# Kernel optimization log

Measured on AMD Instinct MI355X. Metric: run time of the kernel, lower is better.

Reference implementation:

```python
import jax, jax.numpy as jnp
import numpy as np

N_QUBITS = 6
N_LAYERS = 3
DIM = 2 ** N_QUBITS  # 64
BATCH = 262144
FEATURE_DIM = 4
HIDDEN_DIM = 16
N_CLASSES = 4
N_QW = N_LAYERS * N_QUBITS * 3  # 54


def _apply_1q(state, gate, q):
    """Apply a single-qubit gate to qubit q (little-endian: qubit 0 = LSB).
    state: [B, DIM] complex64. gate: [2,2] (shared) or [B,2,2] (per-sample)."""
    B = state.shape[0]
    st = state.reshape(B, 2 ** (N_QUBITS - 1 - q), 2, 2 ** q)
    if gate.ndim == 2:
        out = jnp.einsum('ij,bkjl->bkil', gate, st)
    else:
        out = jnp.einsum('bij,bkjl->bkil', gate, st)
    return out.reshape(B, DIM)


def _cx_perm(c, t):
    # CX(control=c, target=t) is a permutation of basis states: flip bit t where bit c is 1.
    idx = np.arange(DIM)
    return jnp.asarray(idx ^ (((idx >> c) & 1) << t))


def _ry_batched(theta):  # theta: [B] -> [B,2,2]
    c = jnp.cos(theta / 2).astype(jnp.complex64)
    s = jnp.sin(theta / 2).astype(jnp.complex64)
    return jnp.stack([jnp.stack([c, -s], -1), jnp.stack([s, c], -1)], -2)


def _rx(t):  # scalar angle -> [2,2]
    c = jnp.cos(t / 2).astype(jnp.complex64)
    s = jnp.sin(t / 2).astype(jnp.complex64)
    return jnp.stack([jnp.stack([c, -1j * s]), jnp.stack([-1j * s, c])]).astype(jnp.complex64)


def _ry(t):
    c = jnp.cos(t / 2).astype(jnp.complex64)
    s = jnp.sin(t / 2).astype(jnp.complex64)
    return jnp.stack([jnp.stack([c, -s]), jnp.stack([s, c])]).astype(jnp.complex64)


def _rz(t):
    e_m = jnp.exp(-0.5j * t).astype(jnp.complex64)
    e_p = jnp.exp(0.5j * t).astype(jnp.complex64)
    z = jnp.zeros((), jnp.complex64)
    return jnp.stack([jnp.stack([e_m, z]), jnp.stack([z, e_p])])


_H = (jnp.array([[1, 1], [1, -1]], jnp.float32) / np.float32(np.sqrt(2.0))).astype(jnp.complex64)
# signs[s, q] = +1 if bit q of basis state s is 0, else -1  -> Z expectation via probs @ signs
_SIGNS = jnp.asarray(
    1.0 - 2.0 * ((np.arange(DIM)[:, None] >> np.arange(N_QUBITS)[None, :]) & 1),
    dtype=jnp.float32)


def quantum_expectations(angles, qw):
    """Exact batched statevector simulation of the parameterized circuit.
    angles: [B, N_QUBITS] input-encoding RY angles; qw: [N_QW] variational params.
    Returns per-qubit Z expectations [B, N_QUBITS] (exact, i.e. infinite-shot limit)."""
    B = angles.shape[0]
    state = jnp.zeros((B, DIM), jnp.complex64).at[:, 0].set(1.0)
    # Encoding: H then RY(x_q) on each qubit
    for q in range(N_QUBITS):
        state = _apply_1q(state, _H, q)
        state = _apply_1q(state, _ry_batched(angles[:, q]), q)
    # Variational layers
    p = 0
    for _layer in range(N_LAYERS):
        for q in range(N_QUBITS - 1):
            state = state[:, _cx_perm(q, q + 1)]
        for q in range(N_QUBITS):
            state = _apply_1q(state, _rx(qw[p]), q); p += 1
            state = _apply_1q(state, _ry(qw[p]), q); p += 1
            state = _apply_1q(state, _rz(qw[p]), q); p += 1
    probs = state.real ** 2 + state.imag ** 2  # [B, DIM]
    return probs @ _SIGNS  # [B, N_QUBITS]


def setup_inputs() -> dict:
    key = jax.random.key(0)
    ks = jax.random.split(key, 10)
    d = {
        'x': jax.random.normal(ks[0], (BATCH, FEATURE_DIM), jnp.float32),
        'pre_w1': jax.random.normal(ks[1], (FEATURE_DIM, HIDDEN_DIM), jnp.float32) * 0.3,
        'pre_b1': jnp.zeros((HIDDEN_DIM,), jnp.float32),
        'pre_w2': jax.random.normal(ks[2], (HIDDEN_DIM, N_QUBITS), jnp.float32) * 0.2,
        'pre_b2': jnp.zeros((N_QUBITS,), jnp.float32),
        'qw': jax.random.normal(ks[3], (N_QW,), jnp.float32) * 0.1,
        'post_w1': jax.random.normal(ks[4], (N_QUBITS, HIDDEN_DIM), jnp.float32) * 0.3,
        'post_b1': jnp.zeros((HIDDEN_DIM,), jnp.float32),
        'post_w2': jax.random.normal(ks[5], (HIDDEN_DIM, N_CLASSES), jnp.float32) * 0.2,
        'post_b2': jnp.zeros((N_CLASSES,), jnp.float32),
    }
    return d


def reference(x, pre_w1, pre_b1, pre_w2, pre_b2, qw, post_w1, post_b1, post_w2, post_b2):
    # classical_preprocess (dropout is identity in eval): Linear -> ReLU -> Linear -> Tanh
    h = jax.nn.relu(x @ pre_w1 + pre_b1)
    angles = jnp.tanh(h @ pre_w2 + pre_b2)  # [B, N_QUBITS]
    # quantum circuit (original detaches inputs before the circuit -> no grad through it)
    exp = jax.lax.stop_gradient(quantum_expectations(angles, qw))
    # classical_postprocess: Linear -> ReLU -> Linear
    h2 = jax.nn.relu(exp @ post_w1 + post_b1)
    return h2 @ post_w2 + post_b2
```

## Files before the change

### kernel.cpp

```cpp
#include <hip/hip_runtime.h>
#include <math.h>

#define NQ 6
#define NLAYERS 3
#define QBATCH 262144
#define NGATES 18
#define GSTRIDE 40

typedef float  f2   __attribute__((ext_vector_type(2)));
typedef float  f4v  __attribute__((ext_vector_type(4)));
typedef float  f16f __attribute__((ext_vector_type(16)));
typedef __fp16 h2v  __attribute__((ext_vector_type(2)));
typedef __fp16 h8v  __attribute__((ext_vector_type(8)));

__device__ __forceinline__ float lane_swap(float v) {
    return __int_as_float(__builtin_amdgcn_update_dpp(
        0, __float_as_int(v), 0xB1, 0xF, 0xF, true));
}
__device__ __forceinline__ f2 lane_swap2(f2 v) {
    f2 r; r.x = lane_swap(v.x); r.y = lane_swap(v.y); return r;
}
__device__ __forceinline__ float tanh_fast(float a) {
    const float e = __expf(2.f * a);
    return 1.f - 2.f * __builtin_amdgcn_rcpf(e + 1.f);
}

__global__ __launch_bounds__(128) void prep_kernel(
    const float* __restrict__ qw,
    const float* __restrict__ post_w1,
    __fp16* __restrict__ wfrag)
{
    __shared__ f2    gs2[NGATES * GSTRIDE / 2];
    __shared__ float Ure[64][65];
    __shared__ float Uim[64][65];
    const int tid = threadIdx.x;

    if (tid < NGATES) {
        const int pp = tid * 3;
        float s0 = sinf(qw[pp+0]*0.5f), c0 = cosf(qw[pp+0]*0.5f);
        float s1 = sinf(qw[pp+1]*0.5f), c1 = cosf(qw[pp+1]*0.5f);
        float s2 = sinf(qw[pp+2]*0.5f), c2 = cosf(qw[pp+2]*0.5f);
        const float m00r =  c1*c0, m00i =  s1*s0;
        const float m01r = -s1*c0, m01i = -c1*s0;
        const float m10r =  s1*c0, m10i = -c1*s0;
        const float m11r =  c1*c0, m11i = -s1*s0;
        const float g00r = c2*m00r + s2*m00i, g00i = c2*m00i - s2*m00r;
        const float g01r = c2*m01r + s2*m01i, g01i = c2*m01i - s2*m01r;
        const float g10r = c2*m10r - s2*m10i, g10i = c2*m10i + s2*m10r;
        const float g11r = c2*m11r - s2*m11i, g11i = c2*m11i + s2*m11r;
        float* o = (float*)gs2 + tid * GSTRIDE;
        o[0]=o[1]=g00r;  o[2]=o[3]=g00i;  o[4]=o[5]=-g00i;
        o[6]=o[7]=g01r;  o[8]=o[9]=g01i;  o[10]=o[11]=-g01i;
        o[12]=o[13]=g10r; o[14]=o[15]=g10i; o[16]=o[17]=-g10i;
        o[18]=o[19]=g11r; o[20]=o[21]=g11i; o[22]=o[23]=-g11i;
        o[24]=g00r; o[25]=g10r;  o[26]=g00i; o[27]=g10i;
        o[28]=-g00i; o[29]=-g10i; o[30]=g01r; o[31]=g11r;
        o[32]=g01i; o[33]=g11i;  o[34]=-g01i; o[35]=-g11i;
        o[36]=o[37]=o[38]=o[39]=0.f;
    }
    __syncthreads();

    {
        const int bt = tid >> 1, p = tid & 1;
        f2 R[16], U[16];
        #pragma unroll
        for (int j = 0; j < 16; ++j) {
            R[j].x = ((bt >> 5) == p && (bt & 31) == 2*j    ) ? 1.f : 0.f;
            R[j].y = ((bt >> 5) == p && (bt & 31) == 2*j + 1) ? 1.f : 0.f;
            U[j].x = 0.f; U[j].y = 0.f;
        }
        const f2* gpack = gs2;
        #pragma unroll 1
        for (int l = 0; l < NLAYERS; ++l) {
            #pragma unroll
            for (int j = 0; j < 16; j += 2) {
                float t;
                t = R[j].y; R[j].y = R[j+1].y; R[j+1].y = t;
                t = U[j].y; U[j].y = U[j+1].y; U[j+1].y = t;
            }
            #pragma unroll
            for (int c = 1; c < 4; ++c) {
                #pragma unroll
                for (int j = 0; j < 16; ++j) {
                    if (((j >> (c-1)) & 1) && !((j >> c) & 1)) {
                        const int t = j | (1 << c);
                        f2 tmp;
                        tmp = R[j]; R[j] = R[t]; R[t] = tmp;
                        tmp = U[j]; U[j] = U[t]; U[t] = tmp;
                    }
                }
            }
            #pragma unroll
            for (int j = 8; j < 16; ++j) {
                R[j] = lane_swap2(R[j]);
                U[j] = lane_swap2(U[j]);
            }
            const f2* lg = gpack + l * (NQ * (GSTRIDE / 2));
            {
                const f2* gb = lg;
                const f2 A = gb[12], Ai = gb[13], nAi = gb[14];
                const f2 C = gb[15], Ci = gb[16], nCi = gb[17];
                #pragma unroll
                for (int j = 0; j < 16; ++j) {
                    const f2 z = R[j], u = U[j];
                    const f2 br0 = __builtin_shufflevector(z, z, 0, 0);
                    const f2 br1 = __builtin_shufflevector(z, z, 1, 1);
                    const f2 bu0 = __builtin_shufflevector(u, u, 0, 0);
                    const f2 bu1 = __builtin_shufflevector(u, u, 1, 1);
                    R[j] = __builtin_elementwise_fma(nCi, bu1, __builtin_elementwise_fma(C,  br1, __builtin_elementwise_fma(nAi, bu0, A  * br0)));
                    U[j] = __builtin_elementwise_fma(C,   bu1, __builtin_elementwise_fma(Ci, br1, __builtin_elementwise_fma(A,   bu0, Ai * br0)));
                }
            }
            #pragma unroll
            for (int q = 1; q < 5; ++q) {
                const f2* gb = lg + q * (GSTRIDE / 2);
                const f2 a00r = gb[0], a00i = gb[1],  n00i = gb[2];
                const f2 a01r = gb[3], a01i = gb[4],  n01i = gb[5];
                const f2 a10r = gb[6], a10i = gb[7],  n10i = gb[8];
                const f2 a11r = gb[9], a11i = gb[10], n11i = gb[11];
                const int bit = 1 << (q - 1);
                #pragma unroll
                for (int m = 0; m < 8; ++m) {
                    const int ja = ((m >> (q-1)) << q) | (m & (bit - 1));
                    const int jb = ja | bit;
                    const f2 zr0 = R[ja], zu0 = U[ja];
                    const f2 zr1 = R[jb], zu1 = U[jb];
                    R[ja] = __builtin_elementwise_fma(n01i, zu1, __builtin_elementwise_fma(a01r, zr1, __builtin_elementwise_fma(n00i, zu0, a00r * zr0)));
                    U[ja] = __builtin_elementwise_fma(a01r, zu1, __builtin_elementwise_fma(a01i, zr1, __builtin_elementwise_fma(a00r, zu0, a00i * zr0)));
                    R[jb] = __builtin_elementwise_fma(n11i, zu1, __builtin_elementwise_fma(a11r, zr1, __builtin_elementwise_fma(n10i, zu0, a10r * zr0)));
                    U[jb] = __builtin_elementwise_fma(a11r, zu1, __builtin_elementwise_fma(a11i, zr1, __builtin_elementwise_fma(a10r, zu0, a10i * zr0)));
                }
            }
            {
                const f2* gb = lg + 5 * (GSTRIDE / 2);
                const bool sw = (p != 0);
                const f2 rrr  = sw ? gb[9]  : gb[0];
                const f2 rri  = sw ? gb[10] : gb[1];
                const f2 nrri = sw ? gb[11] : gb[2];
                const f2 rpr  = sw ? gb[6]  : gb[3];
                const f2 rpi  = sw ? gb[7]  : gb[4];
                const f2 nrpi = sw ? gb[8]  : gb[5];
                #pragma unroll
                for (int j = 0; j < 16; ++j) {
                    const f2 z = R[j], u = U[j];
                    const f2 pr = lane_swap2(z), pu = lane_swap2(u);
                    R[j] = __builtin_elementwise_fma(nrpi, pu, __builtin_elementwise_fma(rpr, pr, __builtin_elementwise_fma(nrri, u, rrr * z)));
                    U[j] = __builtin_elementwise_fma(rpr,  pu, __builtin_elementwise_fma(rpi, pr, __builtin_elementwise_fma(rrr,  u, rri * z)));
                }
            }
        }
        #pragma unroll
        for (int j = 0; j < 16; ++j) {
            Ure[32*p + 2*j    ][bt] = R[j].x;
            Ure[32*p + 2*j + 1][bt] = R[j].y;
            Uim[32*p + 2*j    ][bt] = U[j].x;
            Uim[32*p + 2*j + 1][bt] = U[j].y;
        }
    }
    __syncthreads();

    {
        const int lane = tid & 63, w = tid >> 6;
        const int r32 = lane & 31, kh = lane >> 5;
        for (int i = w; i < 16; i += 2) {
            const int T = i >> 2, s = i & 3;
            const int row = 32*T + r32, n = row >> 1, cmp = row & 1;
            const float* src = cmp ? &Uim[n][0] : &Ure[n][0];
            h8v v;
            #pragma unroll
            for (int e = 0; e < 8; ++e) v[e] = (__fp16)src[kh*8 + 16*s + e];
            *(h8v*)(wfrag + i*512 + lane*8) = v;
        }
        if (w == 0) {
            const int rlow = lane & 15, kg = lane >> 4;
            float cw[6];
            #pragma unroll
            for (int q = 0; q < 6; ++q) cw[q] = post_w1[q*16 + rlow];
            for (int f = 0; f < 2; ++f) {
                h8v v;
                #pragma unroll
                for (int e = 0; e < 8; ++e) {
                    const int k2 = kg*8 + e + 32*f;
                    float sacc = 0.f;
                    #pragma unroll
                    for (int q = 0; q < 6; ++q)
                        sacc += ((k2 >> q) & 1) ? -cw[q] : cw[q];
                    v[e] = (__fp16)sacc;
                }
                *(h8v*)(wfrag + 8192 + f*512 + lane*8) = v;
            }
        }
    }
}

__global__ __launch_bounds__(256) void qnn_mfma_kernel(
    const float* __restrict__ x,
    const float* __restrict__ pre_w1, const float* __restrict__ pre_b1,
    const float* __restrict__ pre_w2, const float* __restrict__ pre_b2,
    const __fp16* __restrict__ wfrag,
    const float* __restrict__ post_b1, const float* __restrict__ post_w2,
    const float* __restrict__ post_b2,
    float* __restrict__ out)
{
    __shared__ __align__(16) __fp16 ps[4][2048];
    const int tid  = threadIdx.x;
    const int lane = tid & 63, wid = tid >> 6;
    const int sbase = (blockIdx.x * 4 + wid) * 64;

    h8v a1f[16];
    #pragma unroll
    for (int i = 0; i < 16; ++i)
        a1f[i] = *(const h8v*)(wfrag + i*512 + lane*8);
    const h8v a2f0 = *(const h8v*)(wfrag + 8192 + lane*8);
    const h8v a2f1 = *(const h8v*)(wfrag + 8192 + 512 + lane*8);

    const float4 xv = ((const float4*)x)[sbase + lane];
    float h[16];
    #pragma unroll
    for (int j = 0; j < 16; ++j) {
        float a = pre_b1[j];
        a = fmaf(xv.x, pre_w1[0*16+j], a);
        a = fmaf(xv.y, pre_w1[1*16+j], a);
        a = fmaf(xv.z, pre_w1[2*16+j], a);
        a = fmaf(xv.w, pre_w1[3*16+j], a);
        h[j] = fmaxf(a, 0.f);
    }
    float fc[NQ], fs[NQ];
    #pragma unroll
    for (int q = 0; q < NQ; ++q) {
        float a = pre_b2[q];
        #pragma unroll
        for (int j = 0; j < 16; ++j) a = fmaf(h[j], pre_w2[j*NQ+q], a);
        const float y = 0.5f * tanh_fast(a) + 0.78539816339744831f;
        fc[q] = __cosf(y); fs[q] = __sinf(y);
    }
    const float b2x = post_b2[0], b2y = post_b2[1];
    const float b2z = post_b2[2], b2w = post_b2[3];

    const int sl32 = lane & 31, kh = lane >> 5;
    const int sl16 = lane & 15, g2 = lane >> 4;
    __fp16* myp = ps[wid];
    const int wswz = (sl32 & 7) << 4;

    #pragma unroll
    for (int G2 = 0; G2 < 2; ++G2) {
        const int srcb = (G2 * 32 + sl32) << 2;
        #define BP(v) __int_as_float(__builtin_amdgcn_ds_bpermute(srcb, __float_as_int(v)))
        const float q0c=BP(fc[0]), q0s=BP(fs[0]);
        const float q1c=BP(fc[1]), q1s=BP(fs[1]);
        const float q2c=BP(fc[2]), q2s=BP(fs[2]);
        const float q3c=BP(fc[3]), q3s=BP(fs[3]);
        const float q4c=BP(fc[4]), q4s=BP(fs[4]);
        const float q5c=BP(fc[5]), q5s=BP(fs[5]);
        #undef BP
        const float f3v = kh ? q3s : q3c;
        float t01[4], b8[8];
        t01[0] = q0c*q1c; t01[1] = q0s*q1c; t01[2] = q0c*q1s; t01[3] = q0s*q1s;
        #pragma unroll
        for (int e = 0; e < 8; ++e) b8[e] = t01[e & 3] * ((e & 4) ? q2s : q2c);
        h8v bs[4];
        #pragma unroll
        for (int s = 0; s < 4; ++s) {
            const float pre = f3v * ((s & 1) ? q4s : q4c) * ((s & 2) ? q5s : q5c);
            #pragma unroll
            for (int e2 = 0; e2 < 4; ++e2) {
                const h2v t = __builtin_amdgcn_cvt_pkrtz(b8[2*e2]*pre, b8[2*e2+1]*pre);
                bs[s][2*e2] = t[0]; bs[s][2*e2+1] = t[1];
            }
        }

        f16f acc[4];
        #pragma unroll
        for (int T = 0; T < 4; ++T) acc[T] = (f16f)(0.f);
        #pragma unroll
        for (int s = 0; s < 4; ++s) {
            #pragma unroll
            for (int T = 0; T < 4; ++T)
                acc[T] = __builtin_amdgcn_mfma_f32_32x32x16_f16(
                    a1f[T*4 + s], bs[s], acc[T], 0, 0, 0);
        }

        #pragma unroll
        for (int T = 0; T < 4; ++T) {
            #pragma unroll
            for (int a = 0; a < 4; ++a) {
                const float p0 = fmaf(acc[T][4*a+0], acc[T][4*a+0],
                                      acc[T][4*a+1] * acc[T][4*a+1]);
                const float p1 = fmaf(acc[T][4*a+2], acc[T][4*a+2],
                                      acc[T][4*a+3] * acc[T][4*a+3]);
                const h2v ph = __builtin_amdgcn_cvt_pkrtz(p0, p1);
                const int boff = (32*T + 8*a + 4*kh) ^ wswz;
                *(h2v*)((char*)myp + sl32*128 + boff) = ph;
            }
        }

        #pragma unroll
        for (int H = 0; H < 2; ++H) {
            const int smp  = H*16 + sl16;
            const int rswz = (smp & 7) << 4;
            const h8v pb0 = *(const h8v*)((const char*)myp + smp*128 + ((16*g2     ) ^ rswz));
            const h8v pb1 = *(const h8v*)((const char*)myp + smp*128 + ((16*g2 + 64) ^ rswz));
            f4v c2 = {0.f, 0.f, 0.f, 0.f};
            c2 = __builtin_amdgcn_mfma_f32_16x16x32_f16(a2f0, pb0, c2, 0, 0, 0);
            c2 = __builtin_amdgcn_mfma_f32_16x16x32_f16(a2f1, pb1, c2, 0, 0, 0);

            const float4 b1v = ((const float4*)post_b1)[g2];
            const float e0  = fmaxf(c2.x + b1v.x, 0.f);
            const float e1  = fmaxf(c2.y + b1v.y, 0.f);
            const float e2_ = fmaxf(c2.z + b1v.z, 0.f);
            const float e3  = fmaxf(c2.w + b1v.w, 0.f);
            const float4 w0 = ((const float4*)post_w2)[4*g2 + 0];
            const float4 w1 = ((const float4*)post_w2)[4*g2 + 1];
            const float4 w2 = ((const float4*)post_w2)[4*g2 + 2];
            const float4 w3 = ((const float4*)post_w2)[4*g2 + 3];
            float ox = fmaf(e0, w0.x, fmaf(e1, w1.x, fmaf(e2_, w2.x, e3 * w3.x)));
            float oy = fmaf(e0, w0.y, fmaf(e1, w1.y, fmaf(e2_, w2.y, e3 * w3.y)));
            float oz = fmaf(e0, w0.z, fmaf(e1, w1.z, fmaf(e2_, w2.z, e3 * w3.z)));
            float ow = fmaf(e0, w0.w, fmaf(e1, w1.w, fmaf(e2_, w2.w, e3 * w3.w)));
            ox += __shfl_xor(ox, 16, 64); ox += __shfl_xor(ox, 32, 64);
            oy += __shfl_xor(oy, 16, 64); oy += __shfl_xor(oy, 32, 64);
            oz += __shfl_xor(oz, 16, 64); oz += __shfl_xor(oz, 32, 64);
            ow += __shfl_xor(ow, 16, 64); ow += __shfl_xor(ow, 32, 64);
            if (lane < 16) {
                float4 r;
                r.x = ox + b2x; r.y = oy + b2y; r.z = oz + b2z; r.w = ow + b2w;
                ((float4*)out)[sbase + G2*32 + H*16 + sl16] = r;
            }
        }
    }
}

extern "C" void kernel_launch(void* const* d_in, const int* in_sizes, int n_in,
                              void* d_out, int out_size, void* d_ws, size_t ws_size,
                              hipStream_t stream) {
    const float* x       = (const float*)d_in[0];
    const float* pre_w1  = (const float*)d_in[1];
    const float* pre_b1  = (const float*)d_in[2];
    const float* pre_w2  = (const float*)d_in[3];
    const float* pre_b2  = (const float*)d_in[4];
    const float* qw      = (const float*)d_in[5];
    const float* post_w1 = (const float*)d_in[6];
    const float* post_b1 = (const float*)d_in[7];
    const float* post_w2 = (const float*)d_in[8];
    const float* post_b2 = (const float*)d_in[9];
    float* out = (float*)d_out;
    __fp16* wfrag = (__fp16*)d_ws;

    prep_kernel<<<1, 128, 0, stream>>>(qw, post_w1, wfrag);
    qnn_mfma_kernel<<<QBATCH / 256, 256, 0, stream>>>(
        x, pre_w1, pre_b1, pre_w2, pre_b2, wfrag,
        post_b1, post_w2, post_b2, out);
}
```

Baseline: 25.53 us.

## Fuse unitary prep into main kernel, recompute per block with persistent loop

```diff
diff --git a/kernel.cpp b/kernel.cpp
--- a/kernel.cpp
+++ b/kernel.cpp
@@ -25,15 +25,22 @@
     return 1.f - 2.f * __builtin_amdgcn_rcpf(e + 1.f);
 }
 
-__global__ __launch_bounds__(128) void prep_kernel(
+__global__ __launch_bounds__(256) void qnn_fused_all(
+    const float* __restrict__ x,
+    const float* __restrict__ pre_w1, const float* __restrict__ pre_b1,
+    const float* __restrict__ pre_w2, const float* __restrict__ pre_b2,
     const float* __restrict__ qw,
-    const float* __restrict__ post_w1,
-    __fp16* __restrict__ wfrag)
+    const float* __restrict__ post_w1, const float* __restrict__ post_b1,
+    const float* __restrict__ post_w2, const float* __restrict__ post_b2,
+    float* __restrict__ out)
 {
     __shared__ f2    gs2[NGATES * GSTRIDE / 2];
     __shared__ float Ure[64][65];
     __shared__ float Uim[64][65];
-    const int tid = threadIdx.x;
+    __shared__ __align__(16) __fp16 w1s[9216];
+    __shared__ __align__(16) __fp16 ps[4][2048];
+    const int tid  = threadIdx.x;
+    const int lane = tid & 63, wid = tid >> 6;
 
     if (tid < NGATES) {
         const int pp = tid * 3;
@@ -60,7 +67,7 @@
     }
     __syncthreads();
 
-    {
+    if (tid < 128) {
         const int bt = tid >> 1, p = tid & 1;
         f2 R[16], U[16];
         #pragma unroll
@@ -160,18 +167,17 @@
     __syncthreads();
 
     {
-        const int lane = tid & 63, w = tid >> 6;
-        const int r32 = lane & 31, kh = lane >> 5;
-        for (int i = w; i < 16; i += 2) {
+        const int r32 = lane & 31, khp = lane >> 5;
+        for (int i = wid; i < 16; i += 4) {
             const int T = i >> 2, s = i & 3;
             const int row = 32*T + r32, n = row >> 1, cmp = row & 1;
             const float* src = cmp ? &Uim[n][0] : &Ure[n][0];
             h8v v;
             #pragma unroll
-            for (int e = 0; e < 8; ++e) v[e] = (__fp16)src[kh*8 + 16*s + e];
-            *(h8v*)(wfrag + i*512 + lane*8) = v;
-        }
-        if (w == 0) {
+            for (int e = 0; e < 8; ++e) v[e] = (__fp16)src[khp*8 + 16*s + e];
+            *(h8v*)(w1s + i*512 + lane*8) = v;
+        }
+        if (wid == 1) {
             const int rlow = lane & 15, kg = lane >> 4;
             float cw[6];
             #pragma unroll
@@ -187,144 +193,135 @@
                         sacc += ((k2 >> q) & 1) ? -cw[q] : cw[q];
                     v[e] = (__fp16)sacc;
                 }
-                *(h8v*)(wfrag + 8192 + f*512 + lane*8) = v;
+                *(h8v*)(w1s + 8192 + f*512 + lane*8) = v;
             }
         }
     }
-}
-
-__global__ __launch_bounds__(256) void qnn_mfma_kernel(
-    const float* __restrict__ x,
-    const float* __restrict__ pre_w1, const float* __restrict__ pre_b1,
-    const float* __restrict__ pre_w2, const float* __restrict__ pre_b2,
-    const __fp16* __restrict__ wfrag,
-    const float* __restrict__ post_b1, const float* __restrict__ post_w2,
-    const float* __restrict__ post_b2,
-    float* __restrict__ out)
-{
-    __shared__ __align__(16) __fp16 ps[4][2048];
-    const int tid  = threadIdx.x;
-    const int lane = tid & 63, wid = tid >> 6;
-    const int sbase = (blockIdx.x * 4 + wid) * 64;
+    __syncthreads();
 
     h8v a1f[16];
     #pragma unroll
     for (int i = 0; i < 16; ++i)
-        a1f[i] = *(const h8v*)(wfrag + i*512 + lane*8);
-    const h8v a2f0 = *(const h8v*)(wfrag + 8192 + lane*8);
-    const h8v a2f1 = *(const h8v*)(wfrag + 8192 + 512 + lane*8);
-
-    const float4 xv = ((const float4*)x)[sbase + lane];
-    float h[16];
-    #pragma unroll
-    for (int j = 0; j < 16; ++j) {
-        float a = pre_b1[j];
-        a = fmaf(xv.x, pre_w1[0*16+j], a);
-        a = fmaf(xv.y, pre_w1[1*16+j], a);
-        a = fmaf(xv.z, pre_w1[2*16+j], a);
-        a = fmaf(xv.w, pre_w1[3*16+j], a);
-        h[j] = fmaxf(a, 0.f);
-    }
-    float fc[NQ], fs[NQ];
-    #pragma unroll
-    for (int q = 0; q < NQ; ++q) {
-        float a = pre_b2[q];
-        #pragma unroll
-        for (int j = 0; j < 16; ++j) a = fmaf(h[j], pre_w2[j*NQ+q], a);
-        const float y = 0.5f * tanh_fast(a) + 0.78539816339744831f;
-        fc[q] = __cosf(y); fs[q] = __sinf(y);
-    }
+        a1f[i] = *(const h8v*)(w1s + i*512 + lane*8);
+    const h8v a2f0 = *(const h8v*)(w1s + 8192 + lane*8);
+    const h8v a2f1 = *(const h8v*)(w1s + 8192 + 512 + lane*8);
+
     const float b2x = post_b2[0], b2y = post_b2[1];
     const float b2z = post_b2[2], b2w = post_b2[3];
-
     const int sl32 = lane & 31, kh = lane >> 5;
     const int sl16 = lane & 15, g2 = lane >> 4;
     __fp16* myp = ps[wid];
     const int wswz = (sl32 & 7) << 4;
 
-    #pragma unroll
-    for (int G2 = 0; G2 < 2; ++G2) {
-        const int srcb = (G2 * 32 + sl32) << 2;
-        #define BP(v) __int_as_float(__builtin_amdgcn_ds_bpermute(srcb, __float_as_int(v)))
-        const float q0c=BP(fc[0]), q0s=BP(fs[0]);
-        const float q1c=BP(fc[1]), q1s=BP(fs[1]);
-        const float q2c=BP(fc[2]), q2s=BP(fs[2]);
-        const float q3c=BP(fc[3]), q3s=BP(fs[3]);
-        const float q4c=BP(fc[4]), q4s=BP(fs[4]);
-        const float q5c=BP(fc[5]), q5s=BP(fs[5]);
-        #undef BP
-        const float f3v = kh ? q3s : q3c;
-        float t01[4], b8[8];
-        t01[0] = q0c*q1c; t01[1] = q0s*q1c; t01[2] = q0c*q1s; t01[3] = q0s*q1s;
-        #pragma unroll
-        for (int e = 0; e < 8; ++e) b8[e] = t01[e & 3] * ((e & 4) ? q2s : q2c);
-        h8v bs[4];
-        #pragma unroll
-        for (int s = 0; s < 4; ++s) {
-            const float pre = f3v * ((s & 1) ? q4s : q4c) * ((s & 2) ? q5s : q5c);
-            #pragma unroll
-            for (int e2 = 0; e2 < 4; ++e2) {
-                const h2v t = __builtin_amdgcn_cvt_pkrtz(b8[2*e2]*pre, b8[2*e2+1]*pre);
-                bs[s][2*e2] = t[0]; bs[s][2*e2+1] = t[1];
-            }
-        }
-
-        f16f acc[4];
-        #pragma unroll
-        for (int T = 0; T < 4; ++T) acc[T] = (f16f)(0.f);
-        #pragma unroll
-        for (int s = 0; s < 4; ++s) {
-            #pragma unroll
-            for (int T = 0; T < 4; ++T)
-                acc[T] = __builtin_amdgcn_mfma_f32_32x32x16_f16(
-                    a1f[T*4 + s], bs[s], acc[T], 0, 0, 0);
-        }
-
-        #pragma unroll
-        for (int T = 0; T < 4; ++T) {
-            #pragma unroll
-            for (int a = 0; a < 4; ++a) {
-                const float p0 = fmaf(acc[T][4*a+0], acc[T][4*a+0],
-                                      acc[T][4*a+1] * acc[T][4*a+1]);
-                const float p1 = fmaf(acc[T][4*a+2], acc[T][4*a+2],
-                                      acc[T][4*a+3] * acc[T][4*a+3]);
-                const h2v ph = __builtin_amdgcn_cvt_pkrtz(p0, p1);
-                const int boff = (32*T + 8*a + 4*kh) ^ wswz;
-                *(h2v*)((char*)myp + sl32*128 + boff) = ph;
-            }
-        }
-
-        #pragma unroll
-        for (int H = 0; H < 2; ++H) {
-            const int smp  = H*16 + sl16;
-            const int rswz = (smp & 7) << 4;
-            const h8v pb0 = *(const h8v*)((const char*)myp + smp*128 + ((16*g2     ) ^ rswz));
-            const h8v pb1 = *(const h8v*)((const char*)myp + smp*128 + ((16*g2 + 64) ^ rswz));
-            f4v c2 = {0.f, 0.f, 0.f, 0.f};
-            c2 = __builtin_amdgcn_mfma_f32_16x16x32_f16(a2f0, pb0, c2, 0, 0, 0);
-            c2 = __builtin_amdgcn_mfma_f32_16x16x32_f16(a2f1, pb1, c2, 0, 0, 0);
-
-            const float4 b1v = ((const float4*)post_b1)[g2];
-            const float e0  = fmaxf(c2.x + b1v.x, 0.f);
-            const float e1  = fmaxf(c2.y + b1v.y, 0.f);
-            const float e2_ = fmaxf(c2.z + b1v.z, 0.f);
-            const float e3  = fmaxf(c2.w + b1v.w, 0.f);
-            const float4 w0 = ((const float4*)post_w2)[4*g2 + 0];
-            const float4 w1 = ((const float4*)post_w2)[4*g2 + 1];
-            const float4 w2 = ((const float4*)post_w2)[4*g2 + 2];
-            const float4 w3 = ((const float4*)post_w2)[4*g2 + 3];
-            float ox = fmaf(e0, w0.x, fmaf(e1, w1.x, fmaf(e2_, w2.x, e3 * w3.x)));
-            float oy = fmaf(e0, w0.y, fmaf(e1, w1.y, fmaf(e2_, w2.y, e3 * w3.y)));
-            float oz = fmaf(e0, w0.z, fmaf(e1, w1.z, fmaf(e2_, w2.z, e3 * w3.z)));
-            float ow = fmaf(e0, w0.w, fmaf(e1, w1.w, fmaf(e2_, w2.w, e3 * w3.w)));
-            ox += __shfl_xor(ox, 16, 64); ox += __shfl_xor(ox, 32, 64);
-            oy += __shfl_xor(oy, 16, 64); oy += __shfl_xor(oy, 32, 64);
-            oz += __shfl_xor(oz, 16, 64); oz += __shfl_xor(oz, 32, 64);
-            ow += __shfl_xor(ow, 16, 64); ow += __shfl_xor(ow, 32, 64);
-            if (lane < 16) {
-                float4 r;
-                r.x = ox + b2x; r.y = oy + b2y; r.z = oz + b2z; r.w = ow + b2w;
-                ((float4*)out)[sbase + G2*32 + H*16 + sl16] = r;
+    #pragma unroll 1
+    for (int SB = 0; SB < 2; ++SB) {
+        const int sbase = blockIdx.x * 512 + SB * 256 + wid * 64;
+
+        const float4 xv = ((const float4*)x)[sbase + lane];
+        float h[16];
+        #pragma unroll
+        for (int j = 0; j < 16; ++j) {
+            float a = pre_b1[j];
+            a = fmaf(xv.x, pre_w1[0*16+j], a);
+            a = fmaf(xv.y, pre_w1[1*16+j], a);
+            a = fmaf(xv.z, pre_w1[2*16+j], a);
+            a = fmaf(xv.w, pre_w1[3*16+j], a);
+            h[j] = fmaxf(a, 0.f);
+        }
+        float fc[NQ], fs[NQ];
+        #pragma unroll
+        for (int q = 0; q < NQ; ++q) {
+            float a = pre_b2[q];
+            #pragma unroll
+            for (int j = 0; j < 16; ++j) a = fmaf(h[j], pre_w2[j*NQ+q], a);
+            const float y = 0.5f * tanh_fast(a) + 0.78539816339744831f;
+            fc[q] = __cosf(y); fs[q] = __sinf(y);
+        }
+
+        #pragma unroll
+        for (int G2 = 0; G2 < 2; ++G2) {
+            const int srcb = (G2 * 32 + sl32) << 2;
+            #define BP(v) __int_as_float(__builtin_amdgcn_ds_bpermute(srcb, __float_as_int(v)))
+            const float q0c=BP(fc[0]), q0s=BP(fs[0]);
+            const float q1c=BP(fc[1]), q1s=BP(fs[1]);
+            const float q2c=BP(fc[2]), q2s=BP(fs[2]);
+            const float q3c=BP(fc[3]), q3s=BP(fs[3]);
+            const float q4c=BP(fc[4]), q4s=BP(fs[4]);
+            const float q5c=BP(fc[5]), q5s=BP(fs[5]);
+            #undef BP
+            const float f3v = kh ? q3s : q3c;
+            float t01[4], b8[8];
+            t01[0] = q0c*q1c; t01[1] = q0s*q1c; t01[2] = q0c*q1s; t01[3] = q0s*q1s;
+            #pragma unroll
+            for (int e = 0; e < 8; ++e) b8[e] = t01[e & 3] * ((e & 4) ? q2s : q2c);
+            h8v bs[4];
+            #pragma unroll
+            for (int s = 0; s < 4; ++s) {
+                const float pre = f3v * ((s & 1) ? q4s : q4c) * ((s & 2) ? q5s : q5c);
+                #pragma unroll
+                for (int e2 = 0; e2 < 4; ++e2) {
+                    const h2v t = __builtin_amdgcn_cvt_pkrtz(b8[2*e2]*pre, b8[2*e2+1]*pre);
+                    bs[s][2*e2] = t[0]; bs[s][2*e2+1] = t[1];
+                }
+            }
+
+            f16f acc[4];
+            #pragma unroll
+            for (int T = 0; T < 4; ++T) acc[T] = (f16f)(0.f);
+            #pragma unroll
+            for (int s = 0; s < 4; ++s) {
+                #pragma unroll
+                for (int T = 0; T < 4; ++T)
+                    acc[T] = __builtin_amdgcn_mfma_f32_32x32x16_f16(
+                        a1f[T*4 + s], bs[s], acc[T], 0, 0, 0);
+            }
+
+            #pragma unroll
+            for (int T = 0; T < 4; ++T) {
+                #pragma unroll
+                for (int a = 0; a < 4; ++a) {
+                    const float p0 = fmaf(acc[T][4*a+0], acc[T][4*a+0],
+                                          acc[T][4*a+1] * acc[T][4*a+1]);
+                    const float p1 = fmaf(acc[T][4*a+2], acc[T][4*a+2],
+                                          acc[T][4*a+3] * acc[T][4*a+3]);
+                    const h2v ph = __builtin_amdgcn_cvt_pkrtz(p0, p1);
+                    const int boff = (32*T + 8*a + 4*kh) ^ wswz;
+                    *(h2v*)((char*)myp + sl32*128 + boff) = ph;
+                }
+            }
+
+            #pragma unroll
+            for (int H = 0; H < 2; ++H) {
+                const int smp  = H*16 + sl16;
+                const int rswz = (smp & 7) << 4;
+                const h8v pb0 = *(const h8v*)((const char*)myp + smp*128 + ((16*g2     ) ^ rswz));
+                const h8v pb1 = *(const h8v*)((const char*)myp + smp*128 + ((16*g2 + 64) ^ rswz));
+                f4v c2 = {0.f, 0.f, 0.f, 0.f};
+                c2 = __builtin_amdgcn_mfma_f32_16x16x32_f16(a2f0, pb0, c2, 0, 0, 0);
+                c2 = __builtin_amdgcn_mfma_f32_16x16x32_f16(a2f1, pb1, c2, 0, 0, 0);
+
+                const float4 b1v = ((const float4*)post_b1)[g2];
+                const float e0  = fmaxf(c2.x + b1v.x, 0.f);
+                const float e1  = fmaxf(c2.y + b1v.y, 0.f);
+                const float e2_ = fmaxf(c2.z + b1v.z, 0.f);
+                const float e3  = fmaxf(c2.w + b1v.w, 0.f);
+                const float4 w0 = ((const float4*)post_w2)[4*g2 + 0];
+                const float4 w1 = ((const float4*)post_w2)[4*g2 + 1];
+                const float4 w2 = ((const float4*)post_w2)[4*g2 + 2];
+                const float4 w3 = ((const float4*)post_w2)[4*g2 + 3];
+                float ox = fmaf(e0, w0.x, fmaf(e1, w1.x, fmaf(e2_, w2.x, e3 * w3.x)));
+                float oy = fmaf(e0, w0.y, fmaf(e1, w1.y, fmaf(e2_, w2.y, e3 * w3.y)));
+                float oz = fmaf(e0, w0.z, fmaf(e1, w1.z, fmaf(e2_, w2.z, e3 * w3.z)));
+                float ow = fmaf(e0, w0.w, fmaf(e1, w1.w, fmaf(e2_, w2.w, e3 * w3.w)));
+                ox += __shfl_xor(ox, 16, 64); ox += __shfl_xor(ox, 32, 64);
+                oy += __shfl_xor(oy, 16, 64); oy += __shfl_xor(oy, 32, 64);
+                oz += __shfl_xor(oz, 16, 64); oz += __shfl_xor(oz, 32, 64);
+                ow += __shfl_xor(ow, 16, 64); ow += __shfl_xor(ow, 32, 64);
+                if (lane < 16) {
+                    float4 r;
+                    r.x = ox + b2x; r.y = oy + b2y; r.z = oz + b2z; r.w = ow + b2w;
+                    ((float4*)out)[sbase + G2*32 + H*16 + sl16] = r;
+                }
             }
         }
     }
@@ -344,10 +341,8 @@
     const float* post_w2 = (const float*)d_in[8];
     const float* post_b2 = (const float*)d_in[9];
     float* out = (float*)d_out;
-    __fp16* wfrag = (__fp16*)d_ws;
-
-    prep_kernel<<<1, 128, 0, stream>>>(qw, post_w1, wfrag);
-    qnn_mfma_kernel<<<QBATCH / 256, 256, 0, stream>>>(
-        x, pre_w1, pre_b1, pre_w2, pre_b2, wfrag,
-        post_b1, post_w2, post_b2, out);
-}
+
+    qnn_fused_all<<<512, 256, 0, stream>>>(
+        x, pre_w1, pre_b1, pre_w2, pre_b2, qw,
+        post_w1, post_b1, post_w2, post_b2, out);
+}
```

Measured after the change: 36.86 us. +44.4%, slower.
